# Kernel optimization log

Measured on AMD Instinct MI355X. Metric: run time of the kernel, lower is better.

Reference implementation:

```python
import jax, jax.numpy as jnp
import numpy as np
from jax import lax

B, S, C = 128, 512, 16
V, CV = 50000, 100
E, CE = 100, 30
H = 128        # hidden per direction (hidden_dim=256 // 2)
T = 17         # tagset size
NF = 25        # filters per char-conv
LSTM_IN = E + 3 * NF  # 175


def setup_inputs() -> dict:
    key = jax.random.key(0)
    ks = jax.random.split(key, 25)
    sc = 0.1
    inp = {
        "x": jax.random.randint(ks[0], (B, S), 0, V),
        "char_x": jax.random.randint(ks[1], (B, S, C), 0, CV),
        "tags": jax.random.randint(ks[2], (B, S), 0, T),
        "mask": jnp.ones((B, S), dtype=bool),
        "word_emb": jax.random.normal(ks[3], (V, E), jnp.float32) * sc,
        "char_emb": jax.random.normal(ks[4], (CV, CE), jnp.float32) * sc,
        "conv2_W": jax.random.normal(ks[5], (NF, CE, 2), jnp.float32) * sc,
        "conv2_b": jnp.zeros((NF,), jnp.float32),
        "conv3_W": jax.random.normal(ks[6], (NF, CE, 3), jnp.float32) * sc,
        "conv3_b": jnp.zeros((NF,), jnp.float32),
        "conv4_W": jax.random.normal(ks[7], (NF, CE, 4), jnp.float32) * sc,
        "conv4_b": jnp.zeros((NF,), jnp.float32),
        "W_ih_f": jax.random.normal(ks[8], (4 * H, LSTM_IN), jnp.float32) * sc,
        "W_hh_f": jax.random.normal(ks[9], (4 * H, H), jnp.float32) * sc,
        "b_f": jnp.zeros((4 * H,), jnp.float32),
        "W_ih_b": jax.random.normal(ks[10], (4 * H, LSTM_IN), jnp.float32) * sc,
        "W_hh_b": jax.random.normal(ks[11], (4 * H, H), jnp.float32) * sc,
        "b_b": jnp.zeros((4 * H,), jnp.float32),
        "h2t_W": jax.random.normal(ks[12], (T, 2 * H), jnp.float32) * sc,
        "h2t_b": jnp.zeros((T,), jnp.float32),
        "crf_start": jax.random.normal(ks[13], (T,), jnp.float32) * sc,
        "crf_end": jax.random.normal(ks[14], (T,), jnp.float32) * sc,
        "crf_trans": jax.random.normal(ks[15], (T, T), jnp.float32) * sc,
    }
    return inp


def _char_conv(ce, W, b):
    # ce: [BS, CE, C], W: [O, I, K] -> [BS, O] after relu + max-over-time
    out = lax.conv_general_dilated(ce, W, (1,), 'VALID',
                                   dimension_numbers=('NCH', 'OIH', 'NCH'))
    out = jax.nn.relu(out + b[None, :, None])
    return jnp.max(out, axis=-1)


def _lstm_dir(xs, W_ih, W_hh, b, reverse):
    # xs: [B, S, D] -> hs [B, S, H]; PyTorch gate order i,f,g,o
    xs_t = jnp.swapaxes(xs, 0, 1)  # [S, B, D]
    if reverse:
        xs_t = xs_t[::-1]
    pre = jnp.einsum('sbd,gd->sbg', xs_t, W_ih) + b  # hoist input projection
    h0 = jnp.zeros((xs.shape[0], H), xs.dtype)

    def step(carry, p_t):
        h, c = carry
        g = p_t + h @ W_hh.T
        i = jax.nn.sigmoid(g[:, :H])
        f = jax.nn.sigmoid(g[:, H:2 * H])
        gg = jnp.tanh(g[:, 2 * H:3 * H])
        o = jax.nn.sigmoid(g[:, 3 * H:])
        c = f * c + i * gg
        h = o * jnp.tanh(c)
        return (h, c), h

    _, hs = lax.scan(step, (h0, h0), pre)
    if reverse:
        hs = hs[::-1]
    return jnp.swapaxes(hs, 0, 1)


def _crf_nll(emissions, tags, mask, start, end, trans):
    # emissions [B,S,T]; returns sum over batch of -log p(tags | emissions)
    maskf = mask.astype(emissions.dtype)
    # ---- numerator (gold score) ----
    em_sc = jnp.take_along_axis(emissions, tags[..., None], axis=2)[..., 0]  # [B,S]
    tr_sc = trans[tags[:, :-1], tags[:, 1:]]                                  # [B,S-1]
    last_idx = jnp.sum(mask, axis=1).astype(jnp.int32) - 1
    last_tag = tags[jnp.arange(tags.shape[0]), last_idx]
    score = (start[tags[:, 0]] + em_sc[:, 0]
             + jnp.sum(maskf[:, 1:] * (tr_sc + em_sc[:, 1:]), axis=1)
             + end[last_tag])
    # ---- partition via forward-algorithm scan ----
    em_t = jnp.swapaxes(emissions, 0, 1)  # [S,B,T]
    alpha0 = start[None, :] + em_t[0]     # [B,T]

    def step(alpha, inputs):
        e_t, m_t = inputs  # [B,T], [B]
        new = jax.nn.logsumexp(alpha[:, :, None] + trans[None] + e_t[:, None, :], axis=1)
        alpha = jnp.where(m_t[:, None], new, alpha)
        return alpha, None

    alpha, _ = lax.scan(step, alpha0, (em_t[1:], jnp.swapaxes(mask, 0, 1)[1:]))
    logZ = jax.nn.logsumexp(alpha + end[None, :], axis=1)
    return jnp.sum(logZ - score)


def reference(x, char_x, tags, mask, word_emb, char_emb,
              conv2_W, conv2_b, conv3_W, conv3_b, conv4_W, conv4_b,
              W_ih_f, W_hh_f, b_f, W_ih_b, W_hh_b, b_b,
              h2t_W, h2t_b, crf_start, crf_end, crf_trans):
    # word + char features
    we = word_emb[x]                                     # [B,S,E]
    ce = char_emb[char_x].reshape(B * S, C, CE)          # [BS,C,CE]
    ce = jnp.swapaxes(ce, 1, 2)                          # [BS,CE,C]
    cf = jnp.concatenate([_char_conv(ce, conv2_W, conv2_b),
                          _char_conv(ce, conv3_W, conv3_b),
                          _char_conv(ce, conv4_W, conv4_b)], axis=1)
    cf = cf.reshape(B, S, 3 * NF)
    feats = jnp.concatenate([we, cf], axis=2)            # [B,S,175]
    # BiLSTM
    h_fwd = _lstm_dir(feats, W_ih_f, W_hh_f, b_f, reverse=False)
    h_bwd = _lstm_dir(feats, W_ih_b, W_hh_b, b_b, reverse=True)
    h = jnp.concatenate([h_fwd, h_bwd], axis=2)          # [B,S,2H]
    emissions = jnp.einsum('bsh,th->bst', h, h2t_W) + h2t_b
    # CRF NLL (model returns -crf(...), torchcrf reduction='sum')
    return _crf_nll(emissions, tags, mask, crf_start, crf_end, crf_trans)
```

## Files before the change

kernel.cpp:

```cpp
#include <hip/hip_runtime.h>
#include <hip/hip_bf16.h>

#define B_ 128
#define S_ 512
#define C_ 16
#define E_ 100
#define CE_ 30
#define NF_ 25
#define H_ 128
#define T_ 17
#define LSTM_IN_ 175
#define KP_ 192
#define G4_ 512

typedef __hip_bfloat16 bf16;
typedef short bf16x8 __attribute__((ext_vector_type(8)));
typedef float f32x4 __attribute__((ext_vector_type(4)));

__device__ __forceinline__ float bf2f(unsigned short u){
  union { unsigned int i; float f; } v; v.i = ((unsigned int)u) << 16; return v.f;
}
__device__ __forceinline__ float sigm_f(float x){
  float e = __expf(-x);
  return __builtin_amdgcn_rcpf(1.0f + e);
}
__device__ __forceinline__ float tanh_f(float x){
  x = fminf(15.0f, fmaxf(-15.0f, x));
  float e = __expf(-2.0f*x);
  return (1.0f - e) * __builtin_amdgcn_rcpf(1.0f + e);
}

__global__ __launch_bounds__(256) void zero_pad_kernel(bf16* __restrict__ feats){
  int task = blockIdx.x*256 + threadIdx.x;
  int word = task / 17;
  int col = LSTM_IN_ + (task - word*17);
  feats[(size_t)word*KP_ + col] = __float2bfloat16(0.0f);
}

__global__ __launch_bounds__(256) void word_emb_kernel(const int* __restrict__ x,
    const float* __restrict__ wemb, bf16* __restrict__ feats){
  int word = blockIdx.x*2 + (threadIdx.x>>7);
  int e = threadIdx.x & 127;
  if (e < E_) feats[(size_t)word*KP_ + e] = __float2bfloat16(wemb[(size_t)x[word]*E_ + e]);
}

template<int KW>
__global__ __launch_bounds__(256) void char_conv_kernel(const int* __restrict__ char_x,
    const float* __restrict__ cemb, const float* __restrict__ W,
    const float* __restrict__ bias, bf16* __restrict__ feats, int out_off){
  int task = blockIdx.x*256 + threadIdx.x;
  int word = task / NF_;
  int fi = task - word*NF_;
  const int* cx = char_x + word*C_;
  float w[KW*CE_];
  #pragma unroll
  for (int i=0;i<KW*CE_;++i) w[i] = W[fi*CE_*KW + i];
  const int NP = C_ - KW + 1;
  float acc[C_ - KW + 1];
  #pragma unroll
  for (int p=0;p<NP;++p) acc[p] = 0.0f;
  #pragma unroll
  for (int c=0;c<C_;++c){
    int ci = cx[c];
    const float* ce = cemb + ci*CE_;
    #pragma unroll
    for (int e=0;e<CE_;++e){
      float v = ce[e];
      #pragma unroll
      for (int dx=0;dx<KW;++dx){
        int p = c - dx;
        if (p >= 0 && p < NP) acc[p] = fmaf(v, w[e*KW+dx], acc[p]);
      }
    }
  }
  float m = acc[0];
  #pragma unroll
  for (int p=1;p<NP;++p) m = fmaxf(m, acc[p]);
  feats[(size_t)word*KP_ + out_off + fi] = __float2bfloat16(fmaxf(0.0f, m + bias[fi]));
}

__global__ __launch_bounds__(192) void wpack_kernel(const float* __restrict__ Wf,
    const float* __restrict__ Wb, bf16* __restrict__ wpk){
  int g = blockIdx.x;
  int k = threadIdx.x;
  float v = 0.0f;
  if (k < LSTM_IN_) v = (g < 512) ? Wf[g*LSTM_IN_ + k] : Wb[(g-512)*LSTM_IN_ + k];
  wpk[(size_t)g*KP_ + k] = __float2bfloat16(v);
}

__global__ __launch_bounds__(256) void pre_gemm_mfma(const bf16* __restrict__ feats,
    const bf16* __restrict__ wpk, const float* __restrict__ bf_,
    const float* __restrict__ bb_, bf16* __restrict__ pre){
  __shared__ __align__(16) short As[4096];
  __shared__ __align__(16) short Bs[4096];
  int br = blockIdx.x;
  int bc = blockIdx.y;
  int dir = bc >> 2;
  int g0 = (bc & 3) * 128;
  const float* bias = dir ? bb_ : bf_;
  int tid = threadIdx.x;
  int wave = tid >> 6, lane = tid & 63;
  int wr = wave >> 1, wc = wave & 1;
  const bf16* Arow = feats + (size_t)br*128*KP_;
  const bf16* Brow = wpk + (size_t)(dir*512 + g0)*KP_;
  f32x4 acc[4][4];
  #pragma unroll
  for (int i=0;i<4;++i)
    #pragma unroll
    for (int j=0;j<4;++j) acc[i][j] = (f32x4){0.f,0.f,0.f,0.f};

  for (int k0=0; k0<KP_; k0+=32){
    int4 va[2], vb[2];
    #pragma unroll
    for (int hh=0; hh<2; ++hh){
      int slot = tid + hh*256;
      int l = slot & 63;
      int row = ((slot>>6)<<4) + (l & 15);
      int kb = l >> 4;
      va[hh] = *(const int4*)(Arow + row*KP_ + k0 + kb*8);
      vb[hh] = *(const int4*)(Brow + row*KP_ + k0 + kb*8);
    }
    __syncthreads();
    #pragma unroll
    for (int hh=0; hh<2; ++hh){
      int slot = tid + hh*256;
      *(int4*)&As[slot*8] = va[hh];
      *(int4*)&Bs[slot*8] = vb[hh];
    }
    __syncthreads();
    bf16x8 af[4], bfr[4];
    #pragma unroll
    for (int i=0;i<4;++i) af[i]  = *(const bf16x8*)&As[(wr*4+i)*512 + lane*8];
    #pragma unroll
    for (int j=0;j<4;++j) bfr[j] = *(const bf16x8*)&Bs[(wc*4+j)*512 + lane*8];
    #pragma unroll
    for (int i=0;i<4;++i)
      #pragma unroll
      for (int j=0;j<4;++j)
        acc[i][j] = __builtin_amdgcn_mfma_f32_16x16x32_bf16(af[i], bfr[j], acc[i][j], 0, 0, 0);
  }
  int row_l = (lane>>4)*4;
  int col_l = lane & 15;
  float bias_v[4];
  #pragma unroll
  for (int j=0;j<4;++j) bias_v[j] = bias[g0 + wc*64 + j*16 + col_l];
  #pragma unroll
  for (int i=0;i<4;++i){
    #pragma unroll
    for (int q=0;q<4;++q){
      int word = br*128 + wr*64 + i*16 + row_l + q;
      int bidx = word >> 9, sidx = word & 511;
      size_t base = ((size_t)(dir*B_ + bidx)*S_ + sidx)*G4_;
      #pragma unroll
      for (int j=0;j<4;++j){
        int g = g0 + wc*64 + j*16 + col_l;
        pre[base + g] = __float2bfloat16(acc[i][j][q] + bias_v[j]);
      }
    }
  }
}

__global__ __launch_bounds__(512) void lstm_kernel(const bf16* __restrict__ pre,
    const float* __restrict__ Whh_f, const float* __restrict__ Whh_b,
    bf16* __restrict__ hs){
  int blk = blockIdx.x;
  int dir = blk & 1;
  int b = blk >> 1;
  int g = threadIdx.x;
  const float* Whh = dir ? Whh_b : Whh_f;
  float w[128];
  {
    const float* Wrow = Whh + g*H_;
    #pragma unroll
    for (int k4=0;k4<32;++k4){
      float4 v = *(const float4*)&Wrow[k4*4];
      w[4*k4+0]=v.x; w[4*k4+1]=v.y; w[4*k4+2]=v.z; w[4*k4+3]=v.w;
    }
  }
  __shared__ __align__(16) float h_lds[H_];
  __shared__ float gates[G4_];
  if (g < H_) h_lds[g] = 0.0f;
  __syncthreads();
  const bf16* preB = pre + ((size_t)dir*B_ + b)*S_*G4_;
  bf16* hsB = hs + ((size_t)dir*B_ + b)*S_*H_;
  float c = 0.0f;
  int sect = g >> 7;
  float nxt = __bfloat162float(preB[(size_t)(dir ? (S_-1) : 0)*G4_ + g]);
  for (int s=0;s<S_;++s){
    int idx = dir ? (S_-1-s) : s;
    float acc = nxt;
    if (s+1 < S_){
      int idx1 = dir ? (S_-2-s) : (s+1);
      nxt = __bfloat162float(preB[(size_t)idx1*G4_ + g]);
    }
    #pragma unroll
    for (int k4=0;k4<32;++k4){
      float4 h4 = *(const float4*)&h_lds[k4*4];
      acc = fmaf(w[4*k4+0], h4.x, acc);
      acc = fmaf(w[4*k4+1], h4.y, acc);
      acc = fmaf(w[4*k4+2], h4.z, acc);
      acc = fmaf(w[4*k4+3], h4.w, acc);
    }
    float a = (sect == 2) ? tanh_f(acc) : sigm_f(acc);
    gates[g] = a;
    __syncthreads();
    if (g < H_){
      float iv = gates[g];
      float fv = gates[g+128];
      float gv = gates[g+256];
      float ov = gates[g+384];
      c = fmaf(fv, c, iv*gv);
      float hn = ov * tanh_f(c);
      h_lds[g] = hn;
      hsB[(size_t)idx*H_ + g] = __float2bfloat16(hn);
    }
    __syncthreads();
  }
}

__global__ __launch_bounds__(256) void emis_kernel(const bf16* __restrict__ hs,
    const float* __restrict__ W, const float* __restrict__ bias, float* __restrict__ em){
  int task = blockIdx.x*256 + threadIdx.x;
  int word = task / T_;
  int t = task - word*T_;
  const ushort4* hf = (const ushort4*)(hs + (size_t)word*H_);
  const ushort4* hb = (const ushort4*)(hs + (size_t)(B_*S_ + word)*H_);
  const float* w0 = W + t*2*H_;
  float acc = bias[t];
  #pragma unroll
  for (int j4=0;j4<32;++j4){
    ushort4 u = hf[j4];
    float4 w4 = *(const float4*)&w0[j4*4];
    acc = fmaf(bf2f(u.x),w4.x,acc); acc = fmaf(bf2f(u.y),w4.y,acc);
    acc = fmaf(bf2f(u.z),w4.z,acc); acc = fmaf(bf2f(u.w),w4.w,acc);
  }
  #pragma unroll
  for (int j4=0;j4<32;++j4){
    ushort4 u = hb[j4];
    float4 w4 = *(const float4*)&w0[H_ + j4*4];
    acc = fmaf(bf2f(u.x),w4.x,acc); acc = fmaf(bf2f(u.y),w4.y,acc);
    acc = fmaf(bf2f(u.z),w4.z,acc); acc = fmaf(bf2f(u.w),w4.w,acc);
  }
  em[(size_t)word*T_ + t] = acc;
}

__global__ __launch_bounds__(256) void score_kernel(const int* __restrict__ tags,
    const float* __restrict__ em, const float* __restrict__ start,
    const float* __restrict__ end_, const float* __restrict__ trans,
    float* __restrict__ score){
  int b = blockIdx.x;
  int tid = threadIdx.x;
  const int* tg = tags + b*S_;
  const float* eb = em + (size_t)b*S_*T_;
  float s = 0.0f;
  for (int t = tid; t < S_; t += 256){
    int cur = tg[t];
    s += eb[(size_t)t*T_ + cur];
    if (t > 0) s += trans[tg[t-1]*T_ + cur];
  }
  if (tid == 0) s += start[tg[0]] + end_[tg[S_-1]];
  __shared__ float red[256];
  red[tid] = s; __syncthreads();
  for (int off=128; off; off>>=1){
    if (tid < off) red[tid] += red[tid+off];
    __syncthreads();
  }
  if (tid == 0) score[b] = red[0];
}

__global__ __launch_bounds__(64) void crf_alpha_kernel(const float* __restrict__ em,
    const float* __restrict__ start, const float* __restrict__ end_,
    const float* __restrict__ trans, float* __restrict__ logZ){
  int b = blockIdx.x;
  int j = threadIdx.x;
  __shared__ float al[T_];
  const float* eb = em + (size_t)b*S_*T_;
  float tcol[T_];
  if (j < T_){
    #pragma unroll
    for (int i=0;i<T_;++i) tcol[i] = trans[i*T_ + j];
    al[j] = start[j] + eb[j];
  }
  __syncthreads();
  float e_cur = (j < T_) ? eb[T_ + j] : 0.0f;
  for (int s=1;s<S_;++s){
    float e_nxt = (j < T_ && s+1 < S_) ? eb[(size_t)(s+1)*T_ + j] : 0.0f;
    float nv = 0.0f;
    if (j < T_){
      float av[T_];
      float m = -1e30f;
      #pragma unroll
      for (int i=0;i<T_;++i){ av[i] = al[i] + tcol[i]; m = fmaxf(m, av[i]); }
      float sum = 0.0f;
      #pragma unroll
      for (int i=0;i<T_;++i) sum += __expf(av[i]-m);
      nv = m + __logf(sum) + e_cur;
    }
    __syncthreads();
    if (j < T_) al[j] = nv;
    __syncthreads();
    e_cur = e_nxt;
  }
  if (j == 0){
    float m = -1e30f;
    float v[T_];
    #pragma unroll
    for (int i=0;i<T_;++i){ v[i] = al[i] + end_[i]; m = fmaxf(m, v[i]); }
    float sum = 0.0f;
    #pragma unroll
    for (int i=0;i<T_;++i) sum += __expf(v[i]-m);
    logZ[b] = m + __logf(sum);
  }
}

__global__ __launch_bounds__(128) void final_kernel(const float* __restrict__ logZ,
    const float* __restrict__ score, float* __restrict__ out){
  int tid = threadIdx.x;
  float v = logZ[tid] - score[tid];
  __shared__ float red[128];
  red[tid] = v; __syncthreads();
  for (int off=64; off; off>>=1){
    if (tid < off) red[tid] += red[tid+off];
    __syncthreads();
  }
  if (tid == 0) out[0] = red[0];
}

extern "C" void kernel_launch(void* const* d_in, const int* in_sizes, int n_in,
                              void* d_out, int out_size, void* d_ws, size_t ws_size,
                              hipStream_t stream) {
  const int*   x       = (const int*)  d_in[0];
  const int*   char_x  = (const int*)  d_in[1];
  const int*   tags    = (const int*)  d_in[2];
  const float* wemb    = (const float*)d_in[4];
  const float* cemb    = (const float*)d_in[5];
  const float* c2W     = (const float*)d_in[6];
  const float* c2b     = (const float*)d_in[7];
  const float* c3W     = (const float*)d_in[8];
  const float* c3b     = (const float*)d_in[9];
  const float* c4W     = (const float*)d_in[10];
  const float* c4b     = (const float*)d_in[11];
  const float* Wih_f   = (const float*)d_in[12];
  const float* Whh_f   = (const float*)d_in[13];
  const float* b_f     = (const float*)d_in[14];
  const float* Wih_b   = (const float*)d_in[15];
  const float* Whh_b   = (const float*)d_in[16];
  const float* b_b     = (const float*)d_in[17];
  const float* h2tW    = (const float*)d_in[18];
  const float* h2tb    = (const float*)d_in[19];
  const float* crf_s   = (const float*)d_in[20];
  const float* crf_e   = (const float*)d_in[21];
  const float* crf_t   = (const float*)d_in[22];
  float* out = (float*)d_out;

  const size_t NEEDED = 167773184ULL;
  if (ws_size < NEEDED) return;
  char* wsb = (char*)d_ws;
  bf16*  pre   = (bf16*)(wsb);
  bf16*  feats = (bf16*)(wsb + 134217728);
  bf16*  wpk   = (bf16*)(wsb + 159383552);
  bf16*  hs    = (bf16*)(wsb + 134217728);
  float* em    = (float*)(wsb);
  float* score = (float*)(wsb + 167772160);
  float* logZ  = (float*)(wsb + 167772672);

  zero_pad_kernel<<<4352, 256, 0, stream>>>(feats);
  word_emb_kernel<<<32768, 256, 0, stream>>>(x, wemb, feats);
  char_conv_kernel<2><<<6400, 256, 0, stream>>>(char_x, cemb, c2W, c2b, feats, E_);
  char_conv_kernel<3><<<6400, 256, 0, stream>>>(char_x, cemb, c3W, c3b, feats, E_ + NF_);
  char_conv_kernel<4><<<6400, 256, 0, stream>>>(char_x, cemb, c4W, c4b, feats, E_ + 2*NF_);
  wpack_kernel<<<1024, 192, 0, stream>>>(Wih_f, Wih_b, wpk);
  pre_gemm_mfma<<<dim3(512, 8), 256, 0, stream>>>(feats, wpk, b_f, b_b, pre);
  lstm_kernel<<<256, 512, 0, stream>>>(pre, Whh_f, Whh_b, hs);
  emis_kernel<<<4352, 256, 0, stream>>>(hs, h2tW, h2tb, em);
  score_kernel<<<128, 256, 0, stream>>>(tags, em, crf_s, crf_e, crf_t, score);
  crf_alpha_kernel<<<128, 64, 0, stream>>>(em, crf_s, crf_e, crf_t, logZ);
  final_kernel<<<1, 128, 0, stream>>>(logZ, score, out);
}
```

Baseline: 1.655 ms.

## Double-buffer pre-GEMM with direct-to-LDS loads, coalesced stores, split LSTM FMA chain

The input-projection GEMM now stages A/B tiles with global_load_lds into double-buffered shared memory, so the next K-slice loads while the current one is multiplied and one barrier per step is removed. Its epilogue writes results through a swizzled LDS tile and emits 16-byte coalesced global stores instead of scattered 2-byte writes. The LSTM recurrence splits its 128-term dot product into four independent accumulators to shorten the serial FMA dependency chain, and both kernels get occupancy hints in their launch bounds. The cost is more LDS per GEMM block and a slightly different floating-point summation order in the recurrence.

```diff
diff --git a/kernel.cpp b/kernel.cpp
--- a/kernel.cpp
+++ b/kernel.cpp
@@ -29,6 +29,10 @@
   float e = __expf(-2.0f*x);
   return (1.0f - e) * __builtin_amdgcn_rcpf(1.0f + e);
 }
+__device__ __forceinline__ short bf16bits(float f){
+  bf16 b = __float2bfloat16(f);
+  return *(short*)&b;
+}
 
 __global__ __launch_bounds__(256) void zero_pad_kernel(bf16* __restrict__ feats){
   int task = blockIdx.x*256 + threadIdx.x;
@@ -88,11 +92,10 @@
   wpk[(size_t)g*KP_ + k] = __float2bfloat16(v);
 }
 
-__global__ __launch_bounds__(256) void pre_gemm_mfma(const bf16* __restrict__ feats,
+__global__ __launch_bounds__(256, 3) void pre_gemm_mfma(const bf16* __restrict__ feats,
     const bf16* __restrict__ wpk, const float* __restrict__ bf_,
     const float* __restrict__ bb_, bf16* __restrict__ pre){
-  __shared__ __align__(16) short As[4096];
-  __shared__ __align__(16) short Bs[4096];
+  __shared__ __align__(16) short lds[16384];
   int br = blockIdx.x;
   int bc = blockIdx.y;
   int dir = bc >> 2;
@@ -101,46 +104,55 @@
   int tid = threadIdx.x;
   int wave = tid >> 6, lane = tid & 63;
   int wr = wave >> 1, wc = wave & 1;
+  int lrow = lane & 15, lkb = lane >> 4;
   const bf16* Arow = feats + (size_t)br*128*KP_;
   const bf16* Brow = wpk + (size_t)(dir*512 + g0)*KP_;
+
+  auto stage = [&](int bufbase, int k0){
+    int s0 = wave*2, s1 = s0 + 1;
+    __builtin_amdgcn_global_load_lds(
+        (const __attribute__((address_space(1))) void*)(Arow + (size_t)(s0*16 + lrow)*KP_ + k0 + lkb*8),
+        (__attribute__((address_space(3))) void*)&lds[bufbase + s0*512], 16, 0, 0);
+    __builtin_amdgcn_global_load_lds(
+        (const __attribute__((address_space(1))) void*)(Arow + (size_t)(s1*16 + lrow)*KP_ + k0 + lkb*8),
+        (__attribute__((address_space(3))) void*)&lds[bufbase + s1*512], 16, 0, 0);
+    __builtin_amdgcn_global_load_lds(
+        (const __attribute__((address_space(1))) void*)(Brow + (size_t)(s0*16 + lrow)*KP_ + k0 + lkb*8),
+        (__attribute__((address_space(3))) void*)&lds[bufbase + 4096 + s0*512], 16, 0, 0);
+    __builtin_amdgcn_global_load_lds(
+        (const __attribute__((address_space(1))) void*)(Brow + (size_t)(s1*16 + lrow)*KP_ + k0 + lkb*8),
+        (__attribute__((address_space(3))) void*)&lds[bufbase + 4096 + s1*512], 16, 0, 0);
+  };
+
   f32x4 acc[4][4];
   #pragma unroll
   for (int i=0;i<4;++i)
     #pragma unroll
     for (int j=0;j<4;++j) acc[i][j] = (f32x4){0.f,0.f,0.f,0.f};
 
-  for (int k0=0; k0<KP_; k0+=32){
-    int4 va[2], vb[2];
-    #pragma unroll
-    for (int hh=0; hh<2; ++hh){
-      int slot = tid + hh*256;
-      int l = slot & 63;
-      int row = ((slot>>6)<<4) + (l & 15);
-      int kb = l >> 4;
-      va[hh] = *(const int4*)(Arow + row*KP_ + k0 + kb*8);
-      vb[hh] = *(const int4*)(Brow + row*KP_ + k0 + kb*8);
-    }
-    __syncthreads();
-    #pragma unroll
-    for (int hh=0; hh<2; ++hh){
-      int slot = tid + hh*256;
-      *(int4*)&As[slot*8] = va[hh];
-      *(int4*)&Bs[slot*8] = vb[hh];
-    }
-    __syncthreads();
+  stage(0, 0);
+  __syncthreads();
+  int cur = 0;
+  for (int t = 0; t < 6; ++t){
+    if (t < 5) stage((cur^1)*8192, (t+1)*32);
+    const short* A  = &lds[cur*8192];
+    const short* Bv = &lds[cur*8192 + 4096];
     bf16x8 af[4], bfr[4];
     #pragma unroll
-    for (int i=0;i<4;++i) af[i]  = *(const bf16x8*)&As[(wr*4+i)*512 + lane*8];
-    #pragma unroll
-    for (int j=0;j<4;++j) bfr[j] = *(const bf16x8*)&Bs[(wc*4+j)*512 + lane*8];
+    for (int i=0;i<4;++i) af[i]  = *(const bf16x8*)&A[(wr*4+i)*512 + lane*8];
+    #pragma unroll
+    for (int j=0;j<4;++j) bfr[j] = *(const bf16x8*)&Bv[(wc*4+j)*512 + lane*8];
     #pragma unroll
     for (int i=0;i<4;++i)
       #pragma unroll
       for (int j=0;j<4;++j)
         acc[i][j] = __builtin_amdgcn_mfma_f32_16x16x32_bf16(af[i], bfr[j], acc[i][j], 0, 0, 0);
-  }
-  int row_l = (lane>>4)*4;
+    __syncthreads();
+    cur ^= 1;
+  }
+
   int col_l = lane & 15;
+  int row_l = (lane >> 4) * 4;
   float bias_v[4];
   #pragma unroll
   for (int j=0;j<4;++j) bias_v[j] = bias[g0 + wc*64 + j*16 + col_l];
@@ -148,19 +160,29 @@
   for (int i=0;i<4;++i){
     #pragma unroll
     for (int q=0;q<4;++q){
-      int word = br*128 + wr*64 + i*16 + row_l + q;
-      int bidx = word >> 9, sidx = word & 511;
-      size_t base = ((size_t)(dir*B_ + bidx)*S_ + sidx)*G4_;
+      int r = wr*64 + i*16 + row_l + q;
       #pragma unroll
       for (int j=0;j<4;++j){
-        int g = g0 + wc*64 + j*16 + col_l;
-        pre[base + g] = __float2bfloat16(acc[i][j][q] + bias_v[j]);
+        int cbyte = (wc*64 + j*16 + col_l) * 2;
+        int addr = r*256 + (cbyte ^ ((r & 7) << 4));
+        *(short*)((char*)lds + addr) = bf16bits(acc[i][j][q] + bias_v[j]);
       }
     }
   }
-}
-
-__global__ __launch_bounds__(512) void lstm_kernel(const bf16* __restrict__ pre,
+  __syncthreads();
+  int r = tid >> 1, half = tid & 1;
+  int word = br*128 + r;
+  int bidx = word >> 9, sidx = word & 511;
+  bf16* dst = pre + ((size_t)(dir*B_ + bidx)*S_ + sidx)*G4_ + g0 + half*64;
+  #pragma unroll
+  for (int k=0;k<8;++k){
+    int boff = (half*128 + k*16) ^ ((r & 7) << 4);
+    int4 v = *(const int4*)((const char*)lds + r*256 + boff);
+    *(int4*)((char*)dst + k*16) = v;
+  }
+}
+
+__global__ __launch_bounds__(512, 2) void lstm_kernel(const bf16* __restrict__ pre,
     const float* __restrict__ Whh_f, const float* __restrict__ Whh_b,
     bf16* __restrict__ hs){
   int blk = blockIdx.x;
@@ -188,19 +210,21 @@
   float nxt = __bfloat162float(preB[(size_t)(dir ? (S_-1) : 0)*G4_ + g]);
   for (int s=0;s<S_;++s){
     int idx = dir ? (S_-1-s) : s;
-    float acc = nxt;
+    float pr = nxt;
     if (s+1 < S_){
       int idx1 = dir ? (S_-2-s) : (s+1);
       nxt = __bfloat162float(preB[(size_t)idx1*G4_ + g]);
     }
+    float a0=0.f, a1=0.f, a2=0.f, a3=0.f;
     #pragma unroll
     for (int k4=0;k4<32;++k4){
       float4 h4 = *(const float4*)&h_lds[k4*4];
-      acc = fmaf(w[4*k4+0], h4.x, acc);
-      acc = fmaf(w[4*k4+1], h4.y, acc);
-      acc = fmaf(w[4*k4+2], h4.z, acc);
-      acc = fmaf(w[4*k4+3], h4.w, acc);
-    }
+      a0 = fmaf(w[4*k4+0], h4.x, a0);
+      a1 = fmaf(w[4*k4+1], h4.y, a1);
+      a2 = fmaf(w[4*k4+2], h4.z, a2);
+      a3 = fmaf(w[4*k4+3], h4.w, a3);
+    }
+    float acc = pr + ((a0+a1)+(a2+a3));
     float a = (sect == 2) ? tanh_f(acc) : sigm_f(acc);
     gates[g] = a;
     __syncthreads();
```

New measurement: 1.580 ms. 1.05x faster.
